# Performance work log

Measured on AMD Instinct MI355X. Metric: run time of the kernel, lower is better.

Reference implementation:

```python
import jax, jax.numpy as jnp
import numpy as np

B, S, H = 16, 128, 768
L, K = 2, 4
NORM_ITEM = 0.5


def _xavier(key, shape):
    fan_in, fan_out = shape[-1], shape[-2]
    std = float(np.sqrt(2.0 / (fan_in + fan_out)))
    return jax.random.normal(key, shape, dtype=jnp.float32) * std


def setup_inputs() -> dict:
    key = jax.random.key(0)
    ks = jax.random.split(key, 13)
    sentences = jax.random.normal(ks[0], (B, S, H), dtype=jnp.float32)
    adj_matrix = jax.random.uniform(ks[1], (B, K, S, S), dtype=jnp.float32)
    return {
        "sentences": sentences,
        "adj_matrix": adj_matrix,
        # stacked per-(layer, dep_kind) parameters
        "W_in": _xavier(ks[2], (L, K, H, H)),
        "b_in": _xavier(ks[3], (L, K, H, 1)),
        "W_out": _xavier(ks[4], (L, K, H, H)),
        "b_out": _xavier(ks[5], (L, K, H, 1)),
        "Wg_in": _xavier(ks[6], (L, K, H, H)),
        "bg_in": _xavier(ks[7], (L, K, H, 1)),
        "Wg_out": _xavier(ks[8], (L, K, H, H)),
        "bg_out": _xavier(ks[9], (L, K, H, 1)),
        "W_loop": _xavier(ks[10], (L, H, H)),
    }


def reference(sentences, adj_matrix, W_in, b_in, W_out, b_out,
              Wg_in, bg_in, Wg_out, bg_out, W_loop):
    # sentences: [B,S,H], adj_matrix: [B,K,S,S]
    adj_in = adj_matrix                       # message along edges
    adj_out = jnp.swapaxes(adj_matrix, 2, 3)  # reversed edges
    h = jnp.swapaxes(sentences, 1, 2)         # [B,H,S]

    def conv(Wg, bg, W, b, adj, h):
        # Wg,W: [K,H,H]; bg,b: [K,H,1]; adj: [B,K,S,S]; h: [B,H,S]
        gate = jax.nn.sigmoid(jnp.einsum('khd,bds->bkhs', Wg, h) + bg[None])
        rel = NORM_ITEM * gate * (jnp.einsum('khd,bds->bkhs', W, h) + b[None])
        # bmm with adjacency, then sum over dep kinds
        return jnp.einsum('bkhs,bkst->bht', rel, adj)

    n_layers = W_in.shape[0]
    for l in range(n_layers):
        s = jnp.einsum('hd,bds->bhs', W_loop[l], h)  # self loop
        s = s + conv(Wg_in[l], bg_in[l], W_in[l], b_in[l], adj_in, h)
        s = s + conv(Wg_out[l], bg_out[l], W_out[l], b_out[l], adj_out, h)
        h = jax.nn.relu(s)
    return jnp.swapaxes(h, 1, 2)  # [B,S,H]
```

## Files before the change

kernel.cpp:

```cpp
#include <hip/hip_runtime.h>
#include <stdint.h>

#define B_ 16
#define S_ 128
#define H_ 768
#define K_ 4
#define L_ 2
#define T_ (B_*S_)

typedef __attribute__((ext_vector_type(4))) float f32x4;
typedef __attribute__((ext_vector_type(8))) short s16x8;
typedef __bf16 bf16x8 __attribute__((ext_vector_type(8)));
typedef unsigned short u16;

__device__ inline u16 f2bf(float f) {
    union { float f; uint32_t u; } v; v.f = f;
    uint32_t u = v.u;
    return (u16)((u + 0x7fffu + ((u >> 16) & 1u)) >> 16);
}

__device__ inline ushort4 f2bf4(float4 v) {
    ushort4 r; r.x = f2bf(v.x); r.y = f2bf(v.y); r.z = f2bf(v.z); r.w = f2bf(v.w);
    return r;
}

template <typename T>
__device__ inline auto mfma16_impl(T a, T b, f32x4 c, int)
    -> decltype(__builtin_amdgcn_mfma_f32_16x16x32_bf16(a, b, c, 0, 0, 0)) {
    return __builtin_amdgcn_mfma_f32_16x16x32_bf16(a, b, c, 0, 0, 0);
}
template <typename T>
__device__ inline f32x4 mfma16_impl(T a, T b, f32x4 c, long) {
    return __builtin_amdgcn_mfma_f32_16x16x32_bf16(
        __builtin_bit_cast(bf16x8, a), __builtin_bit_cast(bf16x8, b), c, 0, 0, 0);
}
__device__ inline f32x4 mfma16(s16x8 a, s16x8 b, f32x4 c) {
    return mfma16_impl(a, b, c, 0);
}

__device__ inline void gload_lds16(const void* g, void* l) {
    __builtin_amdgcn_global_load_lds(
        (__attribute__((address_space(1))) void*)(g),
        (__attribute__((address_space(3))) void*)(l), 16, 0, 0);
}

__device__ inline void stage128(const char* gRow0, int rowStrideBytes, char* ldsBase, int tid) {
    const int lane = tid & 63;
    const int w = tid >> 6;
    const int lr = lane >> 3;
    #pragma unroll
    for (int j = 0; j < 2; ++j) {
        const int seg = w * 2 + j;
        const int row = seg * 8 + lr;
        const int sb = ((lane & 7) << 4) ^ ((row & 7) << 4);
        gload_lds16(gRow0 + (size_t)row * rowStrideBytes + sb,
                    ldsBase + seg * 1024);
    }
}

__device__ inline void stage_tile(const char* gbase, int rowStrideBytes, u16* lds, int tid) {
    const int lane = tid & 63;
    const int w = tid >> 6;
    const int lr = lane >> 3;
    const int cb = (lane & 7) << 4;
    #pragma unroll
    for (int j = 0; j < 4; ++j) {
        const int seg = j * 4 + w;
        const int row = seg * 8 + lr;
        const int sb = cb ^ ((row & 7) << 4);
        gload_lds16(gbase + (size_t)row * rowStrideBytes + sb, lds + seg * 512);
    }
}

__device__ inline void stage64(const char* gbase, int rowStrideBytes, char* lds, int tid) {
    const int lane = tid & 63;
    const int w = tid >> 6;
    const int lr = lane >> 3;
    const int cb = (lane & 7) << 4;
    #pragma unroll
    for (int j = 0; j < 2; ++j) {
        const int seg = j * 4 + w;
        const int row = seg * 8 + lr;
        const int sb = cb ^ ((row & 7) << 4);
        gload_lds16(gbase + (size_t)row * rowStrideBytes + sb, lds + seg * 1024);
    }
}

__device__ inline s16x8 read_frag(const u16* lds, int row, int colByte) {
    const int bir = colByte ^ ((row & 7) << 4);
    return *(const s16x8*)((const char*)lds + row * 128 + bir);
}

__global__ void prep_weights(const float* __restrict__ Wg_in, const float* __restrict__ Wg_out,
                             const float* __restrict__ W_in,  const float* __restrict__ W_out,
                             const float* __restrict__ W_loop, const float* __restrict__ sent,
                             u16* __restrict__ Wg_all, u16* __restrict__ W_all,
                             u16* __restrict__ Wl, u16* __restrict__ X0) {
    const int i4 = blockIdx.x * blockDim.x + threadIdx.x;
    const int NW4 = L_ * K_ * H_ * H_ / 4;
    const int KHH4 = K_ * H_ * H_ / 4;
    if (i4 < NW4) {
        const int l = i4 / KHH4;
        const int rem = i4 - l * KHH4;
        const int d0 = (l * 2) * KHH4 + rem;
        const int d1 = d0 + KHH4;
        ((ushort4*)Wg_all)[d0] = f2bf4(((const float4*)Wg_in)[i4]);
        ((ushort4*)Wg_all)[d1] = f2bf4(((const float4*)Wg_out)[i4]);
        ((ushort4*)W_all)[d0]  = f2bf4(((const float4*)W_in)[i4]);
        ((ushort4*)W_all)[d1]  = f2bf4(((const float4*)W_out)[i4]);
    }
    if (i4 < L_ * H_ * H_ / 4)  ((ushort4*)Wl)[i4] = f2bf4(((const float4*)W_loop)[i4]);
    if (i4 < T_ * H_ / 4)       ((ushort4*)X0)[i4] = f2bf4(((const float4*)sent)[i4]);
}

__global__ void prep_adj(const float* __restrict__ adj, u16* __restrict__ adjA) {
    const int idx = blockIdx.x * blockDim.x + threadIdx.x;
    const int s = idx & 127;
    const int t = (idx >> 7) & 127;
    const int b = (idx >> 14) & 15;
    const int p = idx >> 18;
    const int dir = p >> 2, k = p & 3;
    const float v = dir ? adj[(((size_t)b * K_ + k) * S_ + t) * S_ + s]
                        : adj[(((size_t)b * K_ + k) * S_ + s) * S_ + t];
    adjA[idx] = f2bf(v);
}

__global__ __launch_bounds__(512, 2)
void gemm1_kernel(const u16* __restrict__ Xb,
                  const u16* __restrict__ Wg_all, const u16* __restrict__ W_all,
                  const float* __restrict__ bg_in, const float* __restrict__ bg_out,
                  const float* __restrict__ b_in,  const float* __restrict__ b_out,
                  int layer, u16* __restrict__ Rel2) {
    __shared__ __align__(16) char smem[98304];

    const int tid = threadIdx.x;
    const int lane = tid & 63;
    const int w = tid >> 6;
    const int wm = w >> 2;
    const int wn = w & 3;
    const int l15 = lane & 15;
    const int hi16 = (lane >> 4) << 4;

    const int bid = blockIdx.x;
    const int p = bid & 7;
    const int g = bid >> 3;
    const int dir = p >> 2, kk = p & 3;
    const size_t woff = ((size_t)(layer * 2 + dir) * K_ + kk) * (size_t)(H_ * H_);

    const char* gAt[3];
    const char* gBrt[3];
    const char* gBgt[3];
    int ys[3], ms[3];
    #pragma unroll
    for (int i = 0; i < 3; ++i) {
        const int task = g * 3 + i;
        const int y = task / 16, m = task % 16;
        ys[i] = y; ms[i] = m;
        gAt[i]  = (const char*)Xb + (size_t)(m * 128) * (H_ * 2);
        gBrt[i] = (const char*)(W_all + woff)  + (size_t)(y * 128) * (H_ * 2);
        gBgt[i] = (const char*)(Wg_all + woff) + (size_t)(y * 128) * (H_ * 2);
    }

    const float* bgp = (dir ? bg_out : bg_in) + ((size_t)layer * K_ + kk) * H_;
    const float* brp = (dir ? b_out  : b_in ) + ((size_t)layer * K_ + kk) * H_;

    auto STAGE = [&](int i, int kt, int c) {
        char* base = smem + c * 49152;
        stage128(gAt[i]  + (size_t)kt * 128, H_ * 2, base, tid);
        stage128(gBrt[i] + (size_t)kt * 128, H_ * 2, base + 16384, tid);
        stage128(gBgt[i] + (size_t)kt * 128, H_ * 2, base + 32768, tid);
    };

    const f32x4 zf = {0.f, 0.f, 0.f, 0.f};
    f32x4 accr[4][2], accg[4][2];
    #pragma unroll
    for (int i = 0; i < 4; ++i)
        #pragma unroll
        for (int j = 0; j < 2; ++j) { accr[i][j] = zf; accg[i][j] = zf; }

    STAGE(0, 0, 0);
    __syncthreads();

    #pragma unroll
    for (int ti = 0; ti < 3; ++ti) {
        for (int kt = 0; kt < 12; ++kt) {
            const int c = kt & 1;
            if (kt < 11)      STAGE(ti, kt + 1, c ^ 1);
            else if (ti < 2)  STAGE(ti + 1, 0, c ^ 1);
            const u16* lA  = (const u16*)(smem + c * 49152);
            const u16* lBr = (const u16*)(smem + c * 49152 + 16384);
            const u16* lBg = (const u16*)(smem + c * 49152 + 32768);
            #pragma unroll
            for (int kq = 0; kq < 2; ++kq) {
                const int ck = kq * 64 + hi16;
                s16x8 a[4], br[2], bg[2];
                #pragma unroll
                for (int i = 0; i < 4; ++i)
                    a[i] = read_frag(lA, wm * 64 + i * 16 + l15, ck);
                #pragma unroll
                for (int j = 0; j < 2; ++j) {
                    br[j] = read_frag(lBr, wn * 32 + j * 16 + l15, ck);
                    bg[j] = read_frag(lBg, wn * 32 + j * 16 + l15, ck);
                }
                #pragma unroll
                for (int i = 0; i < 4; ++i) {
                    #pragma unroll
                    for (int j = 0; j < 2; ++j) {
                        accr[i][j] = mfma16(a[i], br[j], accr[i][j]);
                        accg[i][j] = mfma16(a[i], bg[j], accg[i][j]);
                    }
                }
            }
            __syncthreads();
        }
        {
            const int y = ys[ti], m = ms[ti];
            #pragma unroll
            for (int j = 0; j < 2; ++j) {
                const int h = y * 128 + wn * 32 + j * 16 + l15;
                const float bgv = bgp[h];
                const float brv = brp[h];
                #pragma unroll
                for (int i = 0; i < 4; ++i) {
                    const int tl = wm * 64 + i * 16 + ((lane >> 4) << 2);
                    u16 tmp[4];
                    #pragma unroll
                    for (int rr = 0; rr < 4; ++rr) {
                        const float gv = accg[i][j][rr] + bgv;
                        const float vv = accr[i][j][rr] + brv;
                        tmp[rr] = f2bf(0.5f * vv / (1.f + __expf(-gv)));
                    }
                    ushort4 pk; pk.x = tmp[0]; pk.y = tmp[1]; pk.z = tmp[2]; pk.w = tmp[3];
                    *(ushort4*)(Rel2 + (((size_t)p * B_ + m) * H_ + h) * S_ + tl) = pk;
                    accr[i][j] = zf; accg[i][j] = zf;
                }
            }
        }
    }
}

__global__ __launch_bounds__(256, 2)
void gemm2_kernel(const u16* __restrict__ adjA, const u16* __restrict__ Rel2,
                  const u16* __restrict__ Xc, const u16* __restrict__ Wlb,
                  int layer,
                  u16* __restrict__ Xn, float* __restrict__ Out, int lastLayer) {
    __shared__ __align__(16) char smem2[49152];

    const int tid = threadIdx.x;
    const int lane = tid & 63;
    const int w = tid >> 6;
    const int wm = w >> 1, wn = w & 1;
    const int l15 = lane & 15;
    const int hi16 = (lane >> 4) << 4;
    const int h0 = blockIdx.x * 64;
    const int b = blockIdx.y;

    const char* gX  = (const char*)Xc + ((size_t)b * S_) * (H_ * 2);
    const char* gWl = (const char*)(Wlb + (size_t)layer * H_ * H_) + (size_t)h0 * (H_ * 2);

    auto STAGE = [&](int q, int c) {
        char* base = smem2 + c * 24576;
        if (q < 12) {
            stage_tile(gX + (size_t)q * 128, H_ * 2, (u16*)base, tid);
            stage64(gWl + (size_t)q * 128, H_ * 2, base + 16384, tid);
        } else {
            const int qa = q - 12;
            const int p = qa >> 1, sc = qa & 1;
            const char* Ab = (const char*)adjA + ((size_t)p * B_ + b) * (S_ * S_ * 2) + sc * 128;
            const char* Bb = (const char*)Rel2 + (((size_t)p * B_ + b) * H_ + h0) * (S_ * 2) + sc * 128;
            stage_tile(Ab, S_ * 2, (u16*)base, tid);
            stage64(Bb, S_ * 2, base + 16384, tid);
        }
    };

    const f32x4 zf = {0.f, 0.f, 0.f, 0.f};
    f32x4 acc[4][2];
    #pragma unroll
    for (int i = 0; i < 4; ++i)
        #pragma unroll
        for (int j = 0; j < 2; ++j) acc[i][j] = zf;

    STAGE(0, 0);
    __syncthreads();

    for (int q = 0; q < 28; ++q) {
        const int c = q & 1;
        if (q < 27) STAGE(q + 1, c ^ 1);
        const u16* lA = (const u16*)(smem2 + c * 24576);
        const u16* lB = (const u16*)(smem2 + c * 24576 + 16384);
        #pragma unroll
        for (int kq = 0; kq < 2; ++kq) {
            const int ck = kq * 64 + hi16;
            s16x8 a[4], bb[2];
            #pragma unroll
            for (int i = 0; i < 4; ++i)
                a[i] = read_frag(lA, wm * 64 + i * 16 + l15, ck);
            #pragma unroll
            for (int j = 0; j < 2; ++j)
                bb[j] = read_frag(lB, wn * 32 + j * 16 + l15, ck);
            #pragma unroll
            for (int i = 0; i < 4; ++i)
                #pragma unroll
                for (int j = 0; j < 2; ++j)
                    acc[i][j] = mfma16(a[i], bb[j], acc[i][j]);
        }
        __syncthreads();
    }

    #pragma unroll
    for (int i = 0; i < 4; ++i) {
        const int tl = wm * 64 + i * 16 + ((lane >> 4) << 2);
        #pragma unroll
        for (int j = 0; j < 2; ++j) {
            const int h = h0 + wn * 32 + j * 16 + l15;
            #pragma unroll
            for (int rr = 0; rr < 4; ++rr) {
                const size_t t = (size_t)b * S_ + tl + rr;
                float v = fmaxf(acc[i][j][rr], 0.f);
                if (lastLayer) Out[t * H_ + h] = v;
                else           Xn[t * H_ + h] = f2bf(v);
            }
        }
    }
}

extern "C" void kernel_launch(void* const* d_in, const int* in_sizes, int n_in,
                              void* d_out, int out_size, void* d_ws, size_t ws_size,
                              hipStream_t stream) {
    const float* sent   = (const float*)d_in[0];
    const float* adj    = (const float*)d_in[1];
    const float* W_in   = (const float*)d_in[2];
    const float* b_in   = (const float*)d_in[3];
    const float* W_out  = (const float*)d_in[4];
    const float* b_out  = (const float*)d_in[5];
    const float* Wg_in  = (const float*)d_in[6];
    const float* bg_in  = (const float*)d_in[7];
    const float* Wg_out = (const float*)d_in[8];
    const float* bg_out = (const float*)d_in[9];
    const float* W_loop = (const float*)d_in[10];

    char* ws = (char*)d_ws;
    u16* Wg_all = (u16*)(ws);
    u16* W_all  = (u16*)(ws + 18874368);
    u16* Wlb    = (u16*)(ws + 37748736);
    u16* adjA   = (u16*)(ws + 40108032);
    u16* X0     = (u16*)(ws + 44302336);
    u16* X1     = (u16*)(ws + 47448064);
    u16* Rel2   = (u16*)(ws + 50593792);

    prep_weights<<<4608, 256, 0, stream>>>(Wg_in, Wg_out, W_in, W_out, W_loop, sent,
                                           Wg_all, W_all, Wlb, X0);
    prep_adj<<<8192, 256, 0, stream>>>(adj, adjA);

    u16* Xc = X0;
    u16* Xn = X1;
    for (int l = 0; l < L_; ++l) {
        gemm1_kernel<<<256, 512, 0, stream>>>(Xc, Wg_all, W_all,
                                              bg_in, bg_out, b_in, b_out,
                                              l, Rel2);
        gemm2_kernel<<<dim3(12, 16), 256, 0, stream>>>(adjA, Rel2, Xc, Wlb, l,
                                                       Xn, (float*)d_out, l == L_ - 1);
        u16* t = Xc; Xc = Xn; Xn = t;
    }
}
```

Baseline: 153.3 us.

## Triple-buffer gemm1 LDS staging with prefetch distance two and manual vmcnt waits

```diff
diff --git a/kernel.cpp b/kernel.cpp
--- a/kernel.cpp
+++ b/kernel.cpp
@@ -125,13 +125,13 @@
     adjA[idx] = f2bf(v);
 }
 
-__global__ __launch_bounds__(512, 2)
+__global__ __launch_bounds__(512, 1)
 void gemm1_kernel(const u16* __restrict__ Xb,
                   const u16* __restrict__ Wg_all, const u16* __restrict__ W_all,
                   const float* __restrict__ bg_in, const float* __restrict__ bg_out,
                   const float* __restrict__ b_in,  const float* __restrict__ b_out,
                   int layer, u16* __restrict__ Rel2) {
-    __shared__ __align__(16) char smem[98304];
+    __shared__ __align__(16) char smem[147456];
 
     const int tid = threadIdx.x;
     const int lane = tid & 63;
@@ -146,29 +146,21 @@
     const int g = bid >> 3;
     const int dir = p >> 2, kk = p & 3;
     const size_t woff = ((size_t)(layer * 2 + dir) * K_ + kk) * (size_t)(H_ * H_);
-
-    const char* gAt[3];
-    const char* gBrt[3];
-    const char* gBgt[3];
-    int ys[3], ms[3];
-    #pragma unroll
-    for (int i = 0; i < 3; ++i) {
-        const int task = g * 3 + i;
-        const int y = task / 16, m = task % 16;
-        ys[i] = y; ms[i] = m;
-        gAt[i]  = (const char*)Xb + (size_t)(m * 128) * (H_ * 2);
-        gBrt[i] = (const char*)(W_all + woff)  + (size_t)(y * 128) * (H_ * 2);
-        gBgt[i] = (const char*)(Wg_all + woff) + (size_t)(y * 128) * (H_ * 2);
-    }
+    const char* Wr0 = (const char*)(W_all + woff);
+    const char* Wg0 = (const char*)(Wg_all + woff);
 
     const float* bgp = (dir ? bg_out : bg_in) + ((size_t)layer * K_ + kk) * H_;
     const float* brp = (dir ? b_out  : b_in ) + ((size_t)layer * K_ + kk) * H_;
 
-    auto STAGE = [&](int i, int kt, int c) {
-        char* base = smem + c * 49152;
-        stage128(gAt[i]  + (size_t)kt * 128, H_ * 2, base, tid);
-        stage128(gBrt[i] + (size_t)kt * 128, H_ * 2, base + 16384, tid);
-        stage128(gBgt[i] + (size_t)kt * 128, H_ * 2, base + 32768, tid);
+    auto STAGE_TK = [&](int t2, int k2, int c2) {
+        const int tsk = g * 3 + t2;
+        const int y = tsk >> 4;
+        const int m = tsk & 15;
+        const size_t kb = (size_t)k2 * 128;
+        char* base = smem + c2 * 49152;
+        stage128((const char*)Xb + (size_t)(m * 128) * (H_ * 2) + kb, H_ * 2, base, tid);
+        stage128(Wr0 + (size_t)(y * 128) * (H_ * 2) + kb, H_ * 2, base + 16384, tid);
+        stage128(Wg0 + (size_t)(y * 128) * (H_ * 2) + kb, H_ * 2, base + 32768, tid);
     };
 
     const f32x4 zf = {0.f, 0.f, 0.f, 0.f};
@@ -178,15 +170,24 @@
         #pragma unroll
         for (int j = 0; j < 2; ++j) { accr[i][j] = zf; accg[i][j] = zf; }
 
-    STAGE(0, 0, 0);
-    __syncthreads();
-
-    #pragma unroll
+    STAGE_TK(0, 0, 0);
+    STAGE_TK(0, 1, 1);
+    asm volatile("s_waitcnt vmcnt(6)" ::: "memory");
+    __builtin_amdgcn_s_barrier();
+    __builtin_amdgcn_sched_barrier(0);
+
+    int c = 0;
+    #pragma unroll 1
     for (int ti = 0; ti < 3; ++ti) {
+        #pragma unroll 1
         for (int kt = 0; kt < 12; ++kt) {
-            const int c = kt & 1;
-            if (kt < 11)      STAGE(ti, kt + 1, c ^ 1);
-            else if (ti < 2)  STAGE(ti + 1, 0, c ^ 1);
+            const int vt = ti * 12 + kt;
+            if (vt + 2 < 36) {
+                int t2 = ti, k2 = kt + 2;
+                if (k2 >= 12) { t2 = ti + 1; k2 -= 12; }
+                int c2 = c + 2; if (c2 >= 3) c2 -= 3;
+                STAGE_TK(t2, k2, c2);
+            }
             const u16* lA  = (const u16*)(smem + c * 49152);
             const u16* lBr = (const u16*)(smem + c * 49152 + 16384);
             const u16* lBg = (const u16*)(smem + c * 49152 + 32768);
@@ -202,6 +203,7 @@
                     br[j] = read_frag(lBr, wn * 32 + j * 16 + l15, ck);
                     bg[j] = read_frag(lBg, wn * 32 + j * 16 + l15, ck);
                 }
+                __builtin_amdgcn_s_setprio(1);
                 #pragma unroll
                 for (int i = 0; i < 4; ++i) {
                     #pragma unroll
@@ -210,31 +212,42 @@
                         accg[i][j] = mfma16(a[i], bg[j], accg[i][j]);
                     }
                 }
-            }
-            __syncthreads();
-        }
-        {
-            const int y = ys[ti], m = ms[ti];
-            #pragma unroll
-            for (int j = 0; j < 2; ++j) {
-                const int h = y * 128 + wn * 32 + j * 16 + l15;
-                const float bgv = bgp[h];
-                const float brv = brp[h];
-                #pragma unroll
-                for (int i = 0; i < 4; ++i) {
-                    const int tl = wm * 64 + i * 16 + ((lane >> 4) << 2);
-                    u16 tmp[4];
+                __builtin_amdgcn_s_setprio(0);
+            }
+            if (kt == 11) {
+                const int tsk = g * 3 + ti;
+                const int y = tsk >> 4;
+                const int m = tsk & 15;
+                #pragma unroll
+                for (int j = 0; j < 2; ++j) {
+                    const int h = y * 128 + wn * 32 + j * 16 + l15;
+                    const float bgv = bgp[h];
+                    const float brv = brp[h];
                     #pragma unroll
-                    for (int rr = 0; rr < 4; ++rr) {
-                        const float gv = accg[i][j][rr] + bgv;
-                        const float vv = accr[i][j][rr] + brv;
-                        tmp[rr] = f2bf(0.5f * vv / (1.f + __expf(-gv)));
+                    for (int i = 0; i < 4; ++i) {
+                        const int tl = wm * 64 + i * 16 + ((lane >> 4) << 2);
+                        u16 tmp[4];
+                        #pragma unroll
+                        for (int rr = 0; rr < 4; ++rr) {
+                            const float gv = accg[i][j][rr] + bgv;
+                            const float vv = accr[i][j][rr] + brv;
+                            tmp[rr] = f2bf(0.5f * vv / (1.f + __expf(-gv)));
+                        }
+                        ushort4 pk; pk.x = tmp[0]; pk.y = tmp[1]; pk.z = tmp[2]; pk.w = tmp[3];
+                        *(ushort4*)(Rel2 + (((size_t)p * B_ + m) * H_ + h) * S_ + tl) = pk;
+                        accr[i][j] = zf; accg[i][j] = zf;
                     }
-                    ushort4 pk; pk.x = tmp[0]; pk.y = tmp[1]; pk.z = tmp[2]; pk.w = tmp[3];
-                    *(ushort4*)(Rel2 + (((size_t)p * B_ + m) * H_ + h) * S_ + tl) = pk;
-                    accr[i][j] = zf; accg[i][j] = zf;
                 }
             }
+            if (vt < 35) {
+                if (kt == 11)      asm volatile("s_waitcnt vmcnt(14)" ::: "memory");
+                else if (vt == 34) asm volatile("s_waitcnt vmcnt(0)"  ::: "memory");
+                else               asm volatile("s_waitcnt vmcnt(6)"  ::: "memory");
+                __builtin_amdgcn_sched_barrier(0);
+                __builtin_amdgcn_s_barrier();
+                __builtin_amdgcn_sched_barrier(0);
+            }
+            ++c; if (c == 3) c = 0;
         }
     }
 }
```

Result: slower. 158.5 us (+3.4%).
